# Kernel tuning notes

Hardware: AMD Instinct MI355X
Metric: run time of the kernel (lower is better)

## Reference

```python
import jax, jax.numpy as jnp
import numpy as np

K = 3      # kernel size
S = 1      # stride
P = (K - 1) // 2  # same padding


def setup_inputs() -> dict:
    key = jax.random.key(0)
    k1, k2, k3 = jax.random.split(key, 3)
    x = jax.random.normal(k1, (8, 64, 128, 128), dtype=jnp.float32)
    C2, CIN = 96, 64 * K * K
    # Linear(c1*k^2, c2): weight (c2, c1*k^2), bias (c2,)
    W = jax.random.normal(k2, (C2, CIN), dtype=jnp.float32) / np.sqrt(CIN)
    b = jax.random.normal(k3, (C2,), dtype=jnp.float32) * 0.01
    return {"x": x, "W": W, "b": b}


def _unfold(x):
    # torch nn.Unfold(kernel_size=K, stride=S, padding=P):
    # output (B, C*K*K, L), feature index = c*K*K + ki*K + kj
    B, C, H, Wd = x.shape
    xp = jnp.pad(x, ((0, 0), (0, 0), (P, P), (P, P)))
    Ho = (H + 2 * P - K) // S + 1
    Wo = (Wd + 2 * P - K) // S + 1
    # small fixed K*K loop (9 slices), channel-major ordering matches torch
    patches = jnp.stack(
        [xp[:, :, i:i + (Ho - 1) * S + 1:S, j:j + (Wo - 1) * S + 1:S]
         for i in range(K) for j in range(K)],
        axis=2,
    )  # (B, C, K*K, Ho, Wo)
    return patches.reshape(B, C * K * K, Ho * Wo)


def reference(x, W, b):
    feat = _unfold(x)                      # (B, C*K*K, P)
    feat = jnp.swapaxes(feat, 1, 2)        # (B, P, C*K*K)  == Rearrange 'n c p -> n p c'
    return feat @ W.T + b                  # (B, P, c2)
```

## Files before the change

### kernel.cpp

```cpp
#include <hip/hip_runtime.h>
#include <hip/hip_bf16.h>
#include <stdint.h>


typedef __bf16 bf16t;
typedef __bf16 bf16x8 __attribute__((ext_vector_type(8)));
typedef float  f32x4  __attribute__((ext_vector_type(4)));

#define CIN   64
#define COUT  96
#define HH    128
#define WW    128
#define KTOT  576
#define NCH   18

#define XROW_DW (130 * 32)
#define XTOT_DW (3 * XROW_DW)

__global__ void prep_w_kernel(const float* __restrict__ W, bf16t* __restrict__ Wp) {
    int idx = blockIdx.x * 256 + threadIdx.x;
    if (idx >= NCH * COUT * 32) return;
    int ch  = idx / (COUT * 32);
    int rem = idx - ch * (COUT * 32);
    int n   = rem >> 5;
    int cc  = rem & 31;
    int r = ch >> 1, half = ch & 1;
    Wp[idx] = (bf16t)W[n * KTOT + (half * 32 + cc) * 9 + r];
}

__device__ __forceinline__ int swz(int p) { return ((p >> 2) & 7) ^ ((p & 3) << 1); }

__device__ __forceinline__ uint32_t pack2(float lo, float hi) {
    uint16_t a = __builtin_bit_cast(uint16_t, (__bf16)lo);
    uint16_t b = __builtin_bit_cast(uint16_t, (__bf16)hi);
    return ((uint32_t)b << 16) | (uint32_t)a;
}

__global__ __launch_bounds__(256, 3) void conv_mfma_kernel(
    const float* __restrict__ x, const bf16t* __restrict__ Wp,
    const float* __restrict__ bias, float* __restrict__ out)
{
    __shared__ uint32_t Xs[XTOT_DW];

    const int tid  = threadIdx.x;
    const int lane = tid & 63;
    const int wave = tid >> 6;
    const int lrow = lane & 15;
    const int quad = lane >> 4;
    const int wm   = wave & 1;
    const int wn   = wave >> 1;

    const int bb = blockIdx.x & 7;
    const int oi = blockIdx.x >> 3;

    uint4* X4 = (uint4*)Xs;
    #pragma unroll
    for (int i = 0; i < 13; ++i) {
        int idx = tid + 256 * i;
        if (idx < XTOT_DW / 4) X4[idx] = (uint4){0u, 0u, 0u, 0u};
    }
    __syncthreads();

    const float* xb = x + (size_t)bb * CIN * HH * WW;
    #pragma unroll
    for (int it = 0; it < 12; ++it) {
        int g  = tid + 256 * it;
        int j0 = (g & 31) * 4;
        int cp = (g >> 5) & 31;
        int rh = g >> 10;
        int ii = oi - 1 + rh;
        if ((unsigned)ii < (unsigned)HH) {
            const float* s0 = xb + ((size_t)(2 * cp) * HH + ii) * WW + j0;
            float4 v0 = *(const float4*)s0;
            float4 v1 = *(const float4*)(s0 + HH * WW);
            float e0[4] = {v0.x, v0.y, v0.z, v0.w};
            float e1[4] = {v1.x, v1.y, v1.z, v1.w};
            #pragma unroll
            for (int u = 0; u < 4; ++u) {
                int p   = 1 + j0 + u;
                int cdw = (cp & 3) | ((((cp >> 2) ^ swz(p)) & 7) << 2);
                Xs[rh * XROW_DW + p * 32 + cdw] = pack2(e0[u], e1[u]);
            }
        }
    }
    __syncthreads();

    f32x4 acc[4][3];
    #pragma unroll
    for (int a = 0; a < 4; ++a)
        #pragma unroll
        for (int nt = 0; nt < 3; ++nt)
            acc[a][nt] = (f32x4){0.f, 0.f, 0.f, 0.f};

    int pcol[4];
    #pragma unroll
    for (int a = 0; a < 4; ++a) pcol[a] = wm * 64 + a * 16 + lrow;

    const bf16t* wp_n = Wp + ((size_t)(wn * 48 + lrow)) * 32 + quad * 8;

    for (int r = 0; r < 9; ++r) {
        const int ki = r / 3, kj = r % 3;
        #pragma unroll
        for (int half = 0; half < 2; ++half) {
            const int ch = r * 2 + half;
            bf16x8 bfr[3];
            #pragma unroll
            for (int nt = 0; nt < 3; ++nt)
                bfr[nt] = *(const bf16x8*)(wp_n + (size_t)ch * COUT * 32 + nt * 16 * 32);
            bf16x8 afr[4];
            #pragma unroll
            for (int a = 0; a < 4; ++a) {
                int p   = pcol[a] + kj;
                int blk = (half * 4 + quad) ^ swz(p);
                afr[a] = *(const bf16x8*)&Xs[ki * XROW_DW + p * 32 + blk * 4];
            }
            #pragma unroll
            for (int a = 0; a < 4; ++a)
                #pragma unroll
                for (int nt = 0; nt < 3; ++nt)
                    acc[a][nt] = __builtin_amdgcn_mfma_f32_16x16x32_bf16(
                        afr[a], bfr[nt], acc[a][nt], 0, 0, 0);
        }
    }

    float bv[3];
    #pragma unroll
    for (int nt = 0; nt < 3; ++nt) bv[nt] = bias[wn * 48 + nt * 16 + lrow];

    float* outp = out + ((size_t)bb * 16384 + (size_t)oi * 128) * COUT;
    #pragma unroll
    for (int a = 0; a < 4; ++a) {
        #pragma unroll
        for (int rg = 0; rg < 4; ++rg) {
            int m = wm * 64 + a * 16 + quad * 4 + rg;
            float* rowp = outp + (size_t)m * COUT + wn * 48;
            #pragma unroll
            for (int nt = 0; nt < 3; ++nt)
                rowp[nt * 16 + lrow] = acc[a][nt][rg] + bv[nt];
        }
    }
}

extern "C" void kernel_launch(void* const* d_in, const int* in_sizes, int n_in,
                              void* d_out, int out_size, void* d_ws, size_t ws_size,
                              hipStream_t stream) {
    const float* x    = (const float*)d_in[0];
    const float* W    = (const float*)d_in[1];
    const float* bias = (const float*)d_in[2];
    float* out = (float*)d_out;
    bf16t* Wp  = (bf16t*)d_ws;

    hipLaunchKernelGGL(prep_w_kernel, dim3((NCH * COUT * 32 + 255) / 256), dim3(256), 0, stream,
                       W, Wp);
    hipLaunchKernelGGL(conv_mfma_kernel, dim3(8 * HH), dim3(256), 0, stream,
                       x, Wp, bias, out);
}
```

Measured before the change: 115.6 us.

## Pre-transpose input to padded channel-last bf16 buffer before conv MFMA kernel

Adds a first pass that converts each input row to a zero-padded, channel-last bf16 layout in workspace and also packs the weights. The conv kernel then fills shared memory with contiguous uint4 copies and reads it with a padded stride instead of an XOR swizzle. Blocks grow to 512 threads, with each wave owning fewer M tiles. This moves the strided fp32 gather and conversion, which was repeated three times per row, out of the conv kernel, at the cost of an extra global write and read of the transposed tensor and one more pass.

Result: slower. 122.6 us (+6.0%).

```diff
diff --git a/kernel.cpp b/kernel.cpp
--- a/kernel.cpp
+++ b/kernel.cpp
@@ -13,22 +13,10 @@
 #define WW    128
 #define KTOT  576
 #define NCH   18
+#define PSTR  36
+#define XT_ROW_U4 1040
 
-#define XROW_DW (130 * 32)
-#define XTOT_DW (3 * XROW_DW)
-
-__global__ void prep_w_kernel(const float* __restrict__ W, bf16t* __restrict__ Wp) {
-    int idx = blockIdx.x * 256 + threadIdx.x;
-    if (idx >= NCH * COUT * 32) return;
-    int ch  = idx / (COUT * 32);
-    int rem = idx - ch * (COUT * 32);
-    int n   = rem >> 5;
-    int cc  = rem & 31;
-    int r = ch >> 1, half = ch & 1;
-    Wp[idx] = (bf16t)W[n * KTOT + (half * 32 + cc) * 9 + r];
-}
-
-__device__ __forceinline__ int swz(int p) { return ((p >> 2) & 7) ^ ((p & 3) << 1); }
+__device__ __forceinline__ int swz8(int px) { return ((px >> 2) & 7) ^ ((px & 3) << 1); }
 
 __device__ __forceinline__ uint32_t pack2(float lo, float hi) {
     uint16_t a = __builtin_bit_cast(uint16_t, (__bf16)lo);
@@ -36,90 +24,139 @@
     return ((uint32_t)b << 16) | (uint32_t)a;
 }
 
-__global__ __launch_bounds__(256, 3) void conv_mfma_kernel(
-    const float* __restrict__ x, const bf16t* __restrict__ Wp,
+__global__ __launch_bounds__(256) void pass1_kernel(
+    const float* __restrict__ x, const float* __restrict__ W,
+    bf16t* __restrict__ Wp, uint4* __restrict__ xT)
+{
+    const int tid = threadIdx.x;
+    const int blk = blockIdx.x;
+
+    if (blk >= 1040) {
+        for (int idx = (blk - 1040) * 256 + tid; idx < NCH * COUT * 32; idx += 8 * 256) {
+            int ch  = idx / (COUT * 32);
+            int rem = idx - ch * (COUT * 32);
+            int n = rem >> 5, cc = rem & 31;
+            int r = ch >> 1, half = ch & 1;
+            Wp[idx] = (bf16t)W[n * KTOT + (half * 32 + cc) * 9 + r];
+        }
+        return;
+    }
+
+    __shared__ __align__(16) uint32_t Ls[128 * 32];
+
+    const int b = blk / 130;
+    const int orow = blk - b * 130;
+    uint4* xrow = xT + (size_t)(b * 130 + orow) * XT_ROW_U4;
+
+    if (orow == 0 || orow == 129) {
+        for (int idx = tid; idx < XT_ROW_U4; idx += 256)
+            xrow[idx] = (uint4){0u, 0u, 0u, 0u};
+        return;
+    }
+
+    const int ii = orow - 1;
+    const float* xb = x + (size_t)b * CIN * HH * WW + (size_t)ii * WW;
+
+    #pragma unroll
+    for (int it = 0; it < 4; ++it) {
+        int g  = tid + 256 * it;
+        int j0 = (g & 31) * 4;
+        int cp = g >> 5;
+        const float* s0 = xb + (size_t)(2 * cp) * HH * WW + j0;
+        float4 v0 = *(const float4*)s0;
+        float4 v1 = *(const float4*)(s0 + HH * WW);
+        float e0[4] = {v0.x, v0.y, v0.z, v0.w};
+        float e1[4] = {v1.x, v1.y, v1.z, v1.w};
+        #pragma unroll
+        for (int u = 0; u < 4; ++u) {
+            int px  = j0 + u;
+            int cdw = (cp & 3) | ((((cp >> 2) ^ swz8(px)) & 7) << 2);
+            Ls[px * 32 + cdw] = pack2(e0[u], e1[u]);
+        }
+    }
+    __syncthreads();
+
+    #pragma unroll
+    for (int it = 0; it < 5; ++it) {
+        int idx = tid + 256 * it;
+        if (idx < XT_ROW_U4) {
+            int p = idx >> 3, c = idx & 7;
+            uint4 val;
+            if (p == 0 || p == 129) {
+                val = (uint4){0u, 0u, 0u, 0u};
+            } else {
+                int px = p - 1;
+                val = *(const uint4*)&Ls[px * 32 + ((c ^ swz8(px)) & 7) * 4];
+            }
+            xrow[idx] = val;
+        }
+    }
+}
+
+__global__ __launch_bounds__(512, 4) void conv_kernel(
+    const uint4* __restrict__ xT, const bf16t* __restrict__ Wp,
     const float* __restrict__ bias, float* __restrict__ out)
 {
-    __shared__ uint32_t Xs[XTOT_DW];
+    __shared__ __align__(16) uint32_t Xs[3 * 130 * PSTR];
 
     const int tid  = threadIdx.x;
     const int lane = tid & 63;
     const int wave = tid >> 6;
     const int lrow = lane & 15;
     const int quad = lane >> 4;
-    const int wm   = wave & 1;
-    const int wn   = wave >> 1;
+    const int wn   = wave & 1;
+    const int wm   = wave >> 1;
 
     const int bb = blockIdx.x & 7;
     const int oi = blockIdx.x >> 3;
 
-    uint4* X4 = (uint4*)Xs;
+    const uint4* src = xT + (size_t)(bb * 130 + oi) * XT_ROW_U4;
     #pragma unroll
-    for (int i = 0; i < 13; ++i) {
-        int idx = tid + 256 * i;
-        if (idx < XTOT_DW / 4) X4[idx] = (uint4){0u, 0u, 0u, 0u};
-    }
-    __syncthreads();
-
-    const float* xb = x + (size_t)bb * CIN * HH * WW;
-    #pragma unroll
-    for (int it = 0; it < 12; ++it) {
-        int g  = tid + 256 * it;
-        int j0 = (g & 31) * 4;
-        int cp = (g >> 5) & 31;
-        int rh = g >> 10;
-        int ii = oi - 1 + rh;
-        if ((unsigned)ii < (unsigned)HH) {
-            const float* s0 = xb + ((size_t)(2 * cp) * HH + ii) * WW + j0;
-            float4 v0 = *(const float4*)s0;
-            float4 v1 = *(const float4*)(s0 + HH * WW);
-            float e0[4] = {v0.x, v0.y, v0.z, v0.w};
-            float e1[4] = {v1.x, v1.y, v1.z, v1.w};
-            #pragma unroll
-            for (int u = 0; u < 4; ++u) {
-                int p   = 1 + j0 + u;
-                int cdw = (cp & 3) | ((((cp >> 2) ^ swz(p)) & 7) << 2);
-                Xs[rh * XROW_DW + p * 32 + cdw] = pack2(e0[u], e1[u]);
-            }
+    for (int it = 0; it < 7; ++it) {
+        int s = tid + 512 * it;
+        if (s < 3 * XT_ROW_U4) {
+            int row = s / XT_ROW_U4;
+            int rem = s - row * XT_ROW_U4;
+            int p = rem >> 3, c = rem & 7;
+            *(uint4*)&Xs[(row * 130 + p) * PSTR + c * 4] = src[s];
         }
     }
     __syncthreads();
 
-    f32x4 acc[4][3];
+    f32x4 acc[2][3];
     #pragma unroll
-    for (int a = 0; a < 4; ++a)
+    for (int a = 0; a < 2; ++a)
         #pragma unroll
         for (int nt = 0; nt < 3; ++nt)
             acc[a][nt] = (f32x4){0.f, 0.f, 0.f, 0.f};
 
-    int pcol[4];
-    #pragma unroll
-    for (int a = 0; a < 4; ++a) pcol[a] = wm * 64 + a * 16 + lrow;
+    const bf16t* wp_n = Wp + (size_t)(wn * 48 + lrow) * 32 + quad * 8;
+    const int m0 = wm * 32 + lrow;
 
-    const bf16t* wp_n = Wp + ((size_t)(wn * 48 + lrow)) * 32 + quad * 8;
-
-    for (int r = 0; r < 9; ++r) {
-        const int ki = r / 3, kj = r % 3;
-        #pragma unroll
-        for (int half = 0; half < 2; ++half) {
-            const int ch = r * 2 + half;
-            bf16x8 bfr[3];
+    #pragma unroll 1
+    for (int ki = 0; ki < 3; ++ki) {
+        #pragma unroll 1
+        for (int kj = 0; kj < 3; ++kj) {
             #pragma unroll
-            for (int nt = 0; nt < 3; ++nt)
-                bfr[nt] = *(const bf16x8*)(wp_n + (size_t)ch * COUT * 32 + nt * 16 * 32);
-            bf16x8 afr[4];
-            #pragma unroll
-            for (int a = 0; a < 4; ++a) {
-                int p   = pcol[a] + kj;
-                int blk = (half * 4 + quad) ^ swz(p);
-                afr[a] = *(const bf16x8*)&Xs[ki * XROW_DW + p * 32 + blk * 4];
-            }
-            #pragma unroll
-            for (int a = 0; a < 4; ++a)
+            for (int half = 0; half < 2; ++half) {
+                const int ch = (ki * 3 + kj) * 2 + half;
+                bf16x8 bfr[3];
                 #pragma unroll
                 for (int nt = 0; nt < 3; ++nt)
-                    acc[a][nt] = __builtin_amdgcn_mfma_f32_16x16x32_bf16(
-                        afr[a], bfr[nt], acc[a][nt], 0, 0, 0);
+                    bfr[nt] = *(const bf16x8*)(wp_n + (size_t)ch * COUT * 32 + nt * 512);
+                bf16x8 afr[2];
+                #pragma unroll
+                for (int a = 0; a < 2; ++a) {
+                    int dw = (ki * 130 + m0 + a * 16 + kj) * PSTR + half * 16 + quad * 4;
+                    afr[a] = *(const bf16x8*)&Xs[dw];
+                }
+                #pragma unroll
+                for (int a = 0; a < 2; ++a)
+                    #pragma unroll
+                    for (int nt = 0; nt < 3; ++nt)
+                        acc[a][nt] = __builtin_amdgcn_mfma_f32_16x16x32_bf16(
+                            afr[a], bfr[nt], acc[a][nt], 0, 0, 0);
+            }
         }
     }
 
@@ -127,13 +164,13 @@
     #pragma unroll
     for (int nt = 0; nt < 3; ++nt) bv[nt] = bias[wn * 48 + nt * 16 + lrow];
 
-    float* outp = out + ((size_t)bb * 16384 + (size_t)oi * 128) * COUT;
+    float* outp = out + ((size_t)bb * 16384 + (size_t)oi * 128) * COUT + wn * 48;
     #pragma unroll
-    for (int a = 0; a < 4; ++a) {
+    for (int a = 0; a < 2; ++a) {
         #pragma unroll
         for (int rg = 0; rg < 4; ++rg) {
-            int m = wm * 64 + a * 16 + quad * 4 + rg;
-            float* rowp = outp + (size_t)m * COUT + wn * 48;
+            int m = wm * 32 + a * 16 + quad * 4 + rg;
+            float* rowp = outp + (size_t)m * COUT;
             #pragma unroll
             for (int nt = 0; nt < 3; ++nt)
                 rowp[nt * 16 + lrow] = acc[a][nt][rg] + bv[nt];
@@ -148,10 +185,10 @@
     const float* W    = (const float*)d_in[1];
     const float* bias = (const float*)d_in[2];
     float* out = (float*)d_out;
-    bf16t* Wp  = (bf16t*)d_ws;
 
-    hipLaunchKernelGGL(prep_w_kernel, dim3((NCH * COUT * 32 + 255) / 256), dim3(256), 0, stream,
-                       W, Wp);
-    hipLaunchKernelGGL(conv_mfma_kernel, dim3(8 * HH), dim3(256), 0, stream,
-                       x, Wp, bias, out);
+    bf16t* Wp = (bf16t*)d_ws;
+    uint4* xT = (uint4*)((char*)d_ws + 131072);
+
+    hipLaunchKernelGGL(pass1_kernel, dim3(1048), dim3(256), 0, stream, x, W, Wp, xT);
+    hipLaunchKernelGGL(conv_kernel,  dim3(8 * HH), dim3(512), 0, stream, xT, Wp, bias, out);
 }
```

## Process two output rows per block with 512 threads and prefetch weight fragments

Applied to the files above, without the earlier changes.

Each block now computes two output rows: it stages four input rows in LDS instead of three, uses 8 waves, and launches 512 blocks instead of 1024. This shrinks redundant halo loading (4 rows staged per 2 output rows rather than 3 per 1) and halves block launch overhead. The weight fragments for the next K-chunk are loaded from global memory one iteration ahead, hiding their latency behind the MFMAs. The cost is a larger LDS footprint per block and fewer blocks overall, which may lower occupancy.

New measurement: 109.9 us. -4.9%, faster.

```diff
diff --git a/kernel.cpp b/kernel.cpp
--- a/kernel.cpp
+++ b/kernel.cpp
@@ -13,22 +13,10 @@
 #define WW    128
 #define KTOT  576
 #define NCH   18
+#define XROW  (130 * 32)
+#define XTOT  (4 * XROW)
 
-#define XROW_DW (130 * 32)
-#define XTOT_DW (3 * XROW_DW)
-
-__global__ void prep_w_kernel(const float* __restrict__ W, bf16t* __restrict__ Wp) {
-    int idx = blockIdx.x * 256 + threadIdx.x;
-    if (idx >= NCH * COUT * 32) return;
-    int ch  = idx / (COUT * 32);
-    int rem = idx - ch * (COUT * 32);
-    int n   = rem >> 5;
-    int cc  = rem & 31;
-    int r = ch >> 1, half = ch & 1;
-    Wp[idx] = (bf16t)W[n * KTOT + (half * 32 + cc) * 9 + r];
-}
-
-__device__ __forceinline__ int swz(int p) { return ((p >> 2) & 7) ^ ((p & 3) << 1); }
+__device__ __forceinline__ int swz8(int px) { return ((px >> 2) & 7) ^ ((px & 3) << 1); }
 
 __device__ __forceinline__ uint32_t pack2(float lo, float hi) {
     uint16_t a = __builtin_bit_cast(uint16_t, (__bf16)lo);
@@ -36,39 +24,58 @@
     return ((uint32_t)b << 16) | (uint32_t)a;
 }
 
-__global__ __launch_bounds__(256, 3) void conv_mfma_kernel(
+__global__ __launch_bounds__(256) void prep_w_kernel(
+    const float* __restrict__ W, bf16t* __restrict__ Wp)
+{
+    int idx = blockIdx.x * 256 + threadIdx.x;
+    if (idx >= NCH * COUT * 32) return;
+    int ch  = idx / (COUT * 32);
+    int rem = idx - ch * (COUT * 32);
+    int n = rem >> 5, cc = rem & 31;
+    int r = ch >> 1, half = ch & 1;
+    Wp[idx] = (bf16t)W[n * KTOT + (half * 32 + cc) * 9 + r];
+}
+
+__global__ __launch_bounds__(512, 4) void conv_kernel(
     const float* __restrict__ x, const bf16t* __restrict__ Wp,
     const float* __restrict__ bias, float* __restrict__ out)
 {
-    __shared__ uint32_t Xs[XTOT_DW];
+    __shared__ __align__(16) uint32_t Xs[XTOT];
 
     const int tid  = threadIdx.x;
     const int lane = tid & 63;
     const int wave = tid >> 6;
     const int lrow = lane & 15;
     const int quad = lane >> 4;
-    const int wm   = wave & 1;
-    const int wn   = wave >> 1;
+    const int wn   = wave & 1;
+    const int wm   = wave >> 1;
 
-    const int bb = blockIdx.x & 7;
-    const int oi = blockIdx.x >> 3;
+    const int bb  = blockIdx.x & 7;
+    const int orp = blockIdx.x >> 3;
+
+    const bf16t* wp_n = Wp + (size_t)(wn * 48 + lrow) * 32 + quad * 8;
+
+    bf16x8 bcur[3], bnxt[3];
+    #pragma unroll
+    for (int nt = 0; nt < 3; ++nt)
+        bcur[nt] = *(const bf16x8*)(wp_n + nt * 512);
 
     uint4* X4 = (uint4*)Xs;
     #pragma unroll
-    for (int i = 0; i < 13; ++i) {
-        int idx = tid + 256 * i;
-        if (idx < XTOT_DW / 4) X4[idx] = (uint4){0u, 0u, 0u, 0u};
+    for (int i = 0; i < 9; ++i) {
+        int idx = tid + 512 * i;
+        if (idx < XTOT / 4) X4[idx] = (uint4){0u, 0u, 0u, 0u};
     }
     __syncthreads();
 
     const float* xb = x + (size_t)bb * CIN * HH * WW;
     #pragma unroll
-    for (int it = 0; it < 12; ++it) {
-        int g  = tid + 256 * it;
+    for (int it = 0; it < 8; ++it) {
+        int g  = tid + 512 * it;
         int j0 = (g & 31) * 4;
         int cp = (g >> 5) & 31;
         int rh = g >> 10;
-        int ii = oi - 1 + rh;
+        int ii = orp * 2 - 1 + rh;
         if ((unsigned)ii < (unsigned)HH) {
             const float* s0 = xb + ((size_t)(2 * cp) * HH + ii) * WW + j0;
             float4 v0 = *(const float4*)s0;
@@ -77,9 +84,9 @@
             float e1[4] = {v1.x, v1.y, v1.z, v1.w};
             #pragma unroll
             for (int u = 0; u < 4; ++u) {
-                int p   = 1 + j0 + u;
-                int cdw = (cp & 3) | ((((cp >> 2) ^ swz(p)) & 7) << 2);
-                Xs[rh * XROW_DW + p * 32 + cdw] = pack2(e0[u], e1[u]);
+                int px  = 1 + j0 + u;
+                int cdw = (cp & 3) | ((((cp >> 2) ^ swz8(px)) & 7) << 2);
+                Xs[rh * XROW + px * 32 + cdw] = pack2(e0[u], e1[u]);
             }
         }
     }
@@ -92,48 +99,44 @@
         for (int nt = 0; nt < 3; ++nt)
             acc[a][nt] = (f32x4){0.f, 0.f, 0.f, 0.f};
 
-    int pcol[4];
     #pragma unroll
-    for (int a = 0; a < 4; ++a) pcol[a] = wm * 64 + a * 16 + lrow;
-
-    const bf16t* wp_n = Wp + ((size_t)(wn * 48 + lrow)) * 32 + quad * 8;
-
-    for (int r = 0; r < 9; ++r) {
-        const int ki = r / 3, kj = r % 3;
-        #pragma unroll
-        for (int half = 0; half < 2; ++half) {
-            const int ch = r * 2 + half;
-            bf16x8 bfr[3];
+    for (int ch = 0; ch < NCH; ++ch) {
+        if (ch < NCH - 1) {
             #pragma unroll
             for (int nt = 0; nt < 3; ++nt)
-                bfr[nt] = *(const bf16x8*)(wp_n + (size_t)ch * COUT * 32 + nt * 16 * 32);
-            bf16x8 afr[4];
+                bnxt[nt] = *(const bf16x8*)(wp_n + (size_t)(ch + 1) * 3072 + nt * 512);
+        }
+        const int ki = ch / 6, kj = (ch % 6) >> 1, half = ch & 1;
+        bf16x8 afr[4];
+        #pragma unroll
+        for (int a = 0; a < 4; ++a) {
+            int mb   = wm * 64 + a * 16;
+            int slab = (mb >> 7) + ki;
+            int p    = (mb & 127) + lrow + kj;
+            int blk  = (half * 4 + quad) ^ swz8(p);
+            afr[a] = *(const bf16x8*)&Xs[slab * XROW + p * 32 + blk * 4];
+        }
+        #pragma unroll
+        for (int a = 0; a < 4; ++a)
             #pragma unroll
-            for (int a = 0; a < 4; ++a) {
-                int p   = pcol[a] + kj;
-                int blk = (half * 4 + quad) ^ swz(p);
-                afr[a] = *(const bf16x8*)&Xs[ki * XROW_DW + p * 32 + blk * 4];
-            }
-            #pragma unroll
-            for (int a = 0; a < 4; ++a)
-                #pragma unroll
-                for (int nt = 0; nt < 3; ++nt)
-                    acc[a][nt] = __builtin_amdgcn_mfma_f32_16x16x32_bf16(
-                        afr[a], bfr[nt], acc[a][nt], 0, 0, 0);
-        }
+            for (int nt = 0; nt < 3; ++nt)
+                acc[a][nt] = __builtin_amdgcn_mfma_f32_16x16x32_bf16(
+                    afr[a], bcur[nt], acc[a][nt], 0, 0, 0);
+        #pragma unroll
+        for (int nt = 0; nt < 3; ++nt) bcur[nt] = bnxt[nt];
     }
 
     float bv[3];
     #pragma unroll
     for (int nt = 0; nt < 3; ++nt) bv[nt] = bias[wn * 48 + nt * 16 + lrow];
 
-    float* outp = out + ((size_t)bb * 16384 + (size_t)oi * 128) * COUT;
+    float* outp = out + ((size_t)bb * 16384 + (size_t)orp * 256) * COUT + wn * 48;
     #pragma unroll
     for (int a = 0; a < 4; ++a) {
         #pragma unroll
         for (int rg = 0; rg < 4; ++rg) {
-            int m = wm * 64 + a * 16 + quad * 4 + rg;
-            float* rowp = outp + (size_t)m * COUT + wn * 48;
+            int mm = wm * 64 + a * 16 + quad * 4 + rg;
+            float* rowp = outp + (size_t)mm * COUT;
             #pragma unroll
             for (int nt = 0; nt < 3; ++nt)
                 rowp[nt * 16 + lrow] = acc[a][nt][rg] + bv[nt];
@@ -152,6 +155,6 @@
 
     hipLaunchKernelGGL(prep_w_kernel, dim3((NCH * COUT * 32 + 255) / 256), dim3(256), 0, stream,
                        W, Wp);
-    hipLaunchKernelGGL(conv_mfma_kernel, dim3(8 * HH), dim3(256), 0, stream,
+    hipLaunchKernelGGL(conv_kernel, dim3(512), dim3(512), 0, stream,
                        x, Wp, bias, out);
 }
```
